# Kernel optimization log

Measured on AMD Instinct MI355X. Metric: run time of the kernel, lower is better.

## Reference

```python
import jax, jax.numpy as jnp
import numpy as np

B, C, Q, D = 64, 512, 64, 256  # D = 2 * hidden_size; similarity weight has 3*D = 768 entries


def _length_mask(key, batch, seqlen):
    # realistic padding masks: each row has a random valid prefix length in [seqlen//2, seqlen]
    lens = jax.random.randint(key, (batch,), seqlen // 2, seqlen + 1)
    return (jnp.arange(seqlen)[None, :] < lens[:, None]).astype(jnp.int32)


def setup_inputs() -> dict:
    key = jax.random.key(0)
    k1, k2, k3, k4, k5 = jax.random.split(key, 5)
    context = jax.random.normal(k1, (B, C, D), dtype=jnp.float32)
    question = jax.random.normal(k2, (B, Q, D), dtype=jnp.float32)
    context_mask = _length_mask(k3, B, C)
    question_mask = _length_mask(k4, B, Q)
    w = jax.random.normal(k5, (3 * D,), dtype=jnp.float32) * (1.0 / np.sqrt(3 * D))
    return {"context": context, "question": question,
            "context_mask": context_mask, "question_mask": question_mask, "w": w}


def reference(context, question, context_mask, question_mask, w):
    d = context.shape[-1]
    # Linear([c, q, c*q]) with no bias decomposes exactly into three terms.
    w_c, w_q, w_m = w[:d], w[d:2 * d], w[2 * d:]
    sim = ((context @ w_c)[:, :, None]                      # [B, C, 1]
           + (question @ w_q)[:, None, :]                   # [B, 1, Q]
           + jnp.einsum('bcd,bqd->bcq', context * w_m, question))  # [B, C, Q]
    neg = jnp.finfo(sim.dtype).min
    # context-to-query attention (mask question positions)
    sim_q = jnp.where(question_mask[:, None, :] != 0, sim, neg)
    a = jax.nn.softmax(sim_q, axis=2)                        # [B, C, Q]
    c2q = jnp.einsum('bcq,bqd->bcd', a, question)            # [B, C, D]
    # query-to-context attention (max over Q, mask context positions)
    sim_max = jnp.max(sim, axis=2)                           # [B, C]
    sim_max = jnp.where(context_mask != 0, sim_max, neg)
    b = jax.nn.softmax(sim_max, axis=1)                      # [B, C]
    q2c = jnp.einsum('bc,bcd->bd', b, context)[:, None, :]   # [B, 1, D]
    q2c = jnp.broadcast_to(q2c, context.shape)               # [B, C, D]
    g = jnp.concatenate([context, c2q, context * c2q, context * q2c], axis=-1)
    return g
```

## Files before the change

kernel.cpp:

```cpp
#include <hip/hip_runtime.h>
#include <hip/hip_bf16.h>
#include <float.h>

#define B_ 64
#define C_ 512
#define Q_ 64
#define D_ 256

typedef _Float16 f16x8 __attribute__((ext_vector_type(8)));
typedef float f32x4 __attribute__((ext_vector_type(4)));

union U4H8 { uint4 u; f16x8 h; };
union UH2 { _Float16 h[2]; uint32_t u; };

__device__ __forceinline__ uint32_t packh2(float a, float b) {
  UH2 v; v.h[0] = (_Float16)a; v.h[1] = (_Float16)b; return v.u;
}

__device__ __forceinline__ float wred_sum(float v) {
#pragma unroll
  for (int off = 32; off > 0; off >>= 1) v += __shfl_xor(v, off, 64);
  return v;
}
__device__ __forceinline__ float wred_max(float v) {
#pragma unroll
  for (int off = 32; off > 0; off >>= 1) v = fmaxf(v, __shfl_xor(v, off, 64));
  return v;
}

__global__ __launch_bounds__(256) void k_rowdot(const float* __restrict__ src,
                                                const float* __restrict__ wgt,
                                                float* __restrict__ out, int nrows) {
  int wv = threadIdx.x >> 6, ln = threadIdx.x & 63;
  int row = blockIdx.x * 4 + wv;
  if (row >= nrows) return;
  float4 s4 = *(const float4*)(src + (size_t)row * D_ + 4 * ln);
  float4 w4 = *(const float4*)(wgt + 4 * ln);
  float p = s4.x * w4.x + s4.y * w4.y + s4.z * w4.z + s4.w * w4.w;
  p = wred_sum(p);
  if (ln == 0) out[row] = p;
}

__global__ __launch_bounds__(256, 2) void k_main(
    const float* __restrict__ ctx, const float* __restrict__ qst,
    const int* __restrict__ qmask, const float* __restrict__ w,
    const float* __restrict__ qwq_g, float* __restrict__ g,
    float* __restrict__ simmax_g) {
  __shared__ __align__(16) ushort qraw[Q_ * D_];
  __shared__ __align__(16) ushort qT[D_ * Q_];
  __shared__ __align__(16) ushort pbuf[4][16 * Q_];
  __shared__ float qwq_l[Q_];
  __shared__ int   qml_l[Q_];

  const int bid = blockIdx.x;
  const int b = bid & 63;
  const int c0 = (bid >> 6) * 64;
  const int t = threadIdx.x;
  const int wv = t >> 6, ln = t & 63;
  const int lc = ln & 15;
  const int lg = ln >> 4;
  const int c0w = c0 + wv * 16;

  f16x8 bfrag[8];
  float cwc_p = 0.f;
  const float* crow = ctx + ((size_t)b * C_ + c0w + lc) * D_;
  float* grow0 = g + ((size_t)b * C_ + c0w + lc) * (4 * D_);
#pragma unroll
  for (int kk = 0; kk < 8; ++kk) {
    int kb = kk * 32 + lg * 8;
    float4 cv0 = *(const float4*)(crow + kb);
    float4 cv1 = *(const float4*)(crow + kb + 4);
    float4 wc0 = *(const float4*)(w + kb);
    float4 wc1 = *(const float4*)(w + kb + 4);
    float4 wm0 = *(const float4*)(w + 2 * D_ + kb);
    float4 wm1 = *(const float4*)(w + 2 * D_ + kb + 4);
    cwc_p += cv0.x * wc0.x + cv0.y * wc0.y + cv0.z * wc0.z + cv0.w * wc0.w
           + cv1.x * wc1.x + cv1.y * wc1.y + cv1.z * wc1.z + cv1.w * wc1.w;
    bfrag[kk][0] = (_Float16)(cv0.x * wm0.x);
    bfrag[kk][1] = (_Float16)(cv0.y * wm0.y);
    bfrag[kk][2] = (_Float16)(cv0.z * wm0.z);
    bfrag[kk][3] = (_Float16)(cv0.w * wm0.w);
    bfrag[kk][4] = (_Float16)(cv1.x * wm1.x);
    bfrag[kk][5] = (_Float16)(cv1.y * wm1.y);
    bfrag[kk][6] = (_Float16)(cv1.z * wm1.z);
    bfrag[kk][7] = (_Float16)(cv1.w * wm1.w);
    *(float4*)(grow0 + kb) = cv0;
    *(float4*)(grow0 + kb + 4) = cv1;
  }
  float cwc = cwc_p;
  cwc += __shfl_xor(cwc, 16, 64);
  cwc += __shfl_xor(cwc, 32, 64);

  const float* qb = qst + (size_t)b * Q_ * D_;
#pragma unroll 4
  for (int it = 0; it < 32; ++it) {
    int idx = it * 256 + t;
    int q = idx >> 7, jp = idx & 127;
    float2 v = *(const float2*)(qb + q * D_ + 2 * jp);
    int ch = jp >> 2;
    int phys = (ch & ~7) | ((ch & 7) ^ (q & 7));
    *(uint32_t*)((char*)qraw + q * 512 + phys * 16 + (jp & 3) * 4) = packh2(v.x, v.y);
  }
#pragma unroll 4
  for (int it = 0; it < 32; ++it) {
    int q = t & 63;
    int jp = (t >> 6) + 4 * it;
    float2 v = *(const float2*)(qb + q * D_ + 2 * jp);
    int d0 = 2 * jp, d1 = d0 + 1;
    UH2 h0; h0.h[0] = (_Float16)v.x;
    UH2 h1; h1.h[0] = (_Float16)v.y;
    *(ushort*)((char*)qT + d0 * 128 + (((q >> 3) ^ (d0 & 7)) << 4) + (q & 7) * 2) = (ushort)(h0.u & 0xffff);
    *(ushort*)((char*)qT + d1 * 128 + (((q >> 3) ^ (d1 & 7)) << 4) + (q & 7) * 2) = (ushort)(h1.u & 0xffff);
  }
  if (t < Q_) { qwq_l[t] = qwq_g[b * Q_ + t]; qml_l[t] = qmask[b * Q_ + t]; }
  __syncthreads();

  f32x4 sacc[4];
#pragma unroll
  for (int tq = 0; tq < 4; ++tq) sacc[tq] = f32x4{0.f, 0.f, 0.f, 0.f};
#pragma unroll
  for (int tq = 0; tq < 4; ++tq) {
    int q = 16 * tq + lc;
#pragma unroll
    for (int kk = 0; kk < 8; ++kk) {
      int ch = lg + 4 * kk;
      int phys = (ch & ~7) | ((ch & 7) ^ (q & 7));
      U4H8 a; a.u = *(const uint4*)((const char*)qraw + q * 512 + phys * 16);
      sacc[tq] = __builtin_amdgcn_mfma_f32_16x16x32_f16(a.h, bfrag[kk], sacc[tq], 0, 0, 0);
    }
  }

  float vals[4][4];
  float rmax = -FLT_MAX;
#pragma unroll
  for (int tq = 0; tq < 4; ++tq) {
    float4 qw4 = *(const float4*)(qwq_l + 16 * tq + 4 * lg);
#pragma unroll
    for (int r = 0; r < 4; ++r) {
      float qv = (r == 0) ? qw4.x : (r == 1) ? qw4.y : (r == 2) ? qw4.z : qw4.w;
      vals[tq][r] = sacc[tq][r] + cwc + qv;
      rmax = fmaxf(rmax, vals[tq][r]);
    }
  }
  rmax = fmaxf(rmax, __shfl_xor(rmax, 16, 64));
  rmax = fmaxf(rmax, __shfl_xor(rmax, 32, 64));
  if (ln < 16) simmax_g[b * C_ + c0w + lc] = rmax;

  float mmax = -FLT_MAX;
#pragma unroll
  for (int tq = 0; tq < 4; ++tq) {
    int4 qm4 = *(const int4*)(qml_l + 16 * tq + 4 * lg);
#pragma unroll
    for (int r = 0; r < 4; ++r) {
      int m = (r == 0) ? qm4.x : (r == 1) ? qm4.y : (r == 2) ? qm4.z : qm4.w;
      vals[tq][r] = m ? vals[tq][r] : -FLT_MAX;
      mmax = fmaxf(mmax, vals[tq][r]);
    }
  }
  mmax = fmaxf(mmax, __shfl_xor(mmax, 16, 64));
  mmax = fmaxf(mmax, __shfl_xor(mmax, 32, 64));
  float esum = 0.f;
#pragma unroll
  for (int tq = 0; tq < 4; ++tq)
#pragma unroll
    for (int r = 0; r < 4; ++r) {
      vals[tq][r] = __expf(vals[tq][r] - mmax);
      esum += vals[tq][r];
    }
  esum += __shfl_xor(esum, 16, 64);
  esum += __shfl_xor(esum, 32, 64);
  float inv = 1.f / esum;
#pragma unroll
  for (int tq = 0; tq < 4; ++tq) {
    uint32_t p01 = packh2(vals[tq][0] * inv, vals[tq][1] * inv);
    uint32_t p23 = packh2(vals[tq][2] * inv, vals[tq][3] * inv);
    int qb4 = 16 * tq + 4 * lg;
    int phys = ((qb4 >> 3) ^ (lc & 7));
    char* dst = (char*)pbuf[wv] + lc * 128 + phys * 16 + (qb4 & 7) * 2;
    *(uint2*)dst = uint2{p01, p23};
  }

  f16x8 pfragB[2];
#pragma unroll
  for (int ks = 0; ks < 2; ++ks) {
    int phys = (lg + 4 * ks) ^ (lc & 7);
    U4H8 a; a.u = *(const uint4*)((const char*)pbuf[wv] + lc * 128 + phys * 16);
    pfragB[ks] = a.h;
  }
  const float* crow2 = ctx + ((size_t)b * C_ + c0w + lc) * D_;
  float* grow = g + ((size_t)b * C_ + c0w + lc) * (4 * D_);
#pragma unroll 4
  for (int dt = 0; dt < 16; ++dt) {
    f32x4 acc = f32x4{0.f, 0.f, 0.f, 0.f};
#pragma unroll
    for (int ks = 0; ks < 2; ++ks) {
      int d = dt * 16 + lc;
      int phys = (lg + 4 * ks) ^ (d & 7);
      U4H8 aq; aq.u = *(const uint4*)((const char*)qT + d * 128 + phys * 16);
      acc = __builtin_amdgcn_mfma_f32_16x16x32_f16(aq.h, pfragB[ks], acc, 0, 0, 0);
    }
    int dcol = dt * 16 + 4 * lg;
    float4 cvv = *(const float4*)(crow2 + dcol);
    float4 c2qv{acc[0], acc[1], acc[2], acc[3]};
    *(float4*)(grow + D_ + dcol) = c2qv;
    float4 p2{cvv.x * c2qv.x, cvv.y * c2qv.y, cvv.z * c2qv.z, cvv.w * c2qv.w};
    *(float4*)(grow + 2 * D_ + dcol) = p2;
  }
}

__global__ __launch_bounds__(256) void k_q2c_bs(const float* __restrict__ ctx,
                                                const float* __restrict__ simmax,
                                                const int* __restrict__ cmask,
                                                float* __restrict__ part) {
  int b = blockIdx.x, ch = blockIdx.y, t = threadIdx.x;
  int wv = t >> 6, ln = t & 63;
  __shared__ float bls[C_];
  __shared__ float sred[4];
  __shared__ float ssum[4];
  float v0 = simmax[b * C_ + t], v1 = simmax[b * C_ + 256 + t];
  if (!cmask[b * C_ + t]) v0 = -FLT_MAX;
  if (!cmask[b * C_ + 256 + t]) v1 = -FLT_MAX;
  float mx = wred_max(fmaxf(v0, v1));
  if (ln == 0) sred[wv] = mx;
  __syncthreads();
  float bm = fmaxf(fmaxf(sred[0], sred[1]), fmaxf(sred[2], sred[3]));
  float e0 = __expf(v0 - bm), e1 = __expf(v1 - bm);
  float ps = wred_sum(e0 + e1);
  if (ln == 0) ssum[wv] = ps;
  __syncthreads();
  float bs = ssum[0] + ssum[1] + ssum[2] + ssum[3];
  float invbs = 1.f / bs;
  bls[t] = e0 * invbs;
  bls[256 + t] = e1 * invbs;
  __syncthreads();
  float acc = 0.f;
  int cbeg = ch * 64;
#pragma unroll 4
  for (int c = cbeg; c < cbeg + 64; ++c)
    acc += bls[c] * ctx[((size_t)b * C_ + c) * D_ + t];
  part[((size_t)b * 8 + ch) * D_ + t] = acc;
}

__global__ __launch_bounds__(256) void k_g3q(const float* __restrict__ ctx,
                                             const float* __restrict__ part,
                                             float* __restrict__ g) {
  int b = blockIdx.x, ch = blockIdx.y, t = threadIdx.x;
  __shared__ float q2c_l[D_];
  float s = 0.f;
#pragma unroll
  for (int k = 0; k < 8; ++k) s += part[((size_t)b * 8 + k) * D_ + t];
  q2c_l[t] = s;
  __syncthreads();
  int d4 = t & 63;
  int ro = t >> 6;
  float4 qv = *(const float4*)(q2c_l + 4 * d4);
#pragma unroll 4
  for (int it = 0; it < 16; ++it) {
    int c = ch * 64 + it * 4 + ro;
    float4 cv = *(const float4*)(ctx + ((size_t)b * C_ + c) * D_ + 4 * d4);
    float4 o{cv.x * qv.x, cv.y * qv.y, cv.z * qv.z, cv.w * qv.w};
    *(float4*)(g + ((size_t)b * C_ + c) * (4 * D_) + 3 * D_ + 4 * d4) = o;
  }
}

extern "C" void kernel_launch(void* const* d_in, const int* in_sizes, int n_in,
                              void* d_out, int out_size, void* d_ws, size_t ws_size,
                              hipStream_t stream) {
  const float* ctx   = (const float*)d_in[0];
  const float* qst   = (const float*)d_in[1];
  const int*   cmask = (const int*)d_in[2];
  const int*   qmask = (const int*)d_in[3];
  const float* w     = (const float*)d_in[4];
  float* g  = (float*)d_out;
  float* ws = (float*)d_ws;

  float* qwq    = ws;
  float* simmax = ws + 4096;
  float* part   = ws + 36864;

  k_rowdot<<<dim3(B_ * Q_ / 4), 256, 0, stream>>>(qst, w + D_, qwq, B_ * Q_);
  k_main<<<dim3(512), 256, 0, stream>>>(ctx, qst, qmask, w, qwq, g, simmax);
  k_q2c_bs<<<dim3(B_, 8), 256, 0, stream>>>(ctx, simmax, cmask, part);
  k_g3q<<<dim3(B_, 8), 256, 0, stream>>>(ctx, part, g);
}
```

Baseline: 66.41 us.

## Prepack swizzled fp16 question tiles once per batch and DMA them into LDS

```diff
diff --git a/kernel.cpp b/kernel.cpp
--- a/kernel.cpp
+++ b/kernel.cpp
@@ -41,11 +41,59 @@
   if (ln == 0) out[row] = p;
 }
 
+__global__ __launch_bounds__(512) void k_prepack(const float* __restrict__ qst,
+                                                 const float* __restrict__ w,
+                                                 uint32_t* __restrict__ qraw_img,
+                                                 uint32_t* __restrict__ qT_img,
+                                                 float* __restrict__ qwq) {
+  const int b = blockIdx.x;
+  const int t = threadIdx.x;
+  const float* qb = qst + (size_t)b * Q_ * D_;
+#pragma unroll
+  for (int it = 0; it < 16; ++it) {
+    int idx = it * 512 + t;
+    int q = idx >> 7, jp = idx & 127;
+    float2 v = *(const float2*)(qb + q * D_ + 2 * jp);
+    int ch = jp >> 2;
+    int phys = (ch & ~7) | ((ch & 7) ^ (q & 7));
+    qraw_img[(size_t)b * 8192 + q * 128 + phys * 4 + (jp & 3)] = packh2(v.x, v.y);
+  }
+  if (t < 256) {
+    int d = t;
+    uint32_t* dst = qT_img + (size_t)b * 8192 + d * 32;
+#pragma unroll
+    for (int qc = 0; qc < 8; ++qc) {
+      uint32_t tmp[4];
+#pragma unroll
+      for (int e = 0; e < 4; ++e) {
+        int q0 = qc * 8 + e * 2;
+        tmp[e] = packh2(qb[q0 * D_ + d], qb[(q0 + 1) * D_ + d]);
+      }
+      int pc = qc ^ (d & 7);
+      *(uint4*)(dst + pc * 4) = uint4{tmp[0], tmp[1], tmp[2], tmp[3]};
+    }
+  } else {
+    int q = (t - 256) >> 2, sl = t & 3;
+    float p = 0.f;
+#pragma unroll
+    for (int i = 0; i < 16; ++i) {
+      float4 v = *(const float4*)(qb + q * D_ + sl * 64 + i * 4);
+      float4 ww = *(const float4*)(w + D_ + sl * 64 + i * 4);
+      p += v.x * ww.x + v.y * ww.y + v.z * ww.z + v.w * ww.w;
+    }
+    p += __shfl_xor(p, 1, 64);
+    p += __shfl_xor(p, 2, 64);
+    if (sl == 0) qwq[b * Q_ + q] = p;
+  }
+}
+
+template<int IMG>
 __global__ __launch_bounds__(256, 2) void k_main(
     const float* __restrict__ ctx, const float* __restrict__ qst,
     const int* __restrict__ qmask, const float* __restrict__ w,
-    const float* __restrict__ qwq_g, float* __restrict__ g,
-    float* __restrict__ simmax_g) {
+    const float* __restrict__ qwq_g,
+    const uint32_t* __restrict__ qraw_img, const uint32_t* __restrict__ qT_img,
+    float* __restrict__ g, float* __restrict__ simmax_g) {
   __shared__ __align__(16) ushort qraw[Q_ * D_];
   __shared__ __align__(16) ushort qT[D_ * Q_];
   __shared__ __align__(16) ushort pbuf[4][16 * Q_];
@@ -60,6 +108,23 @@
   const int lc = ln & 15;
   const int lg = ln >> 4;
   const int c0w = c0 + wv * 16;
+
+  if constexpr (IMG) {
+    const uint32_t* qr_src = qraw_img + (size_t)b * 8192;
+    const uint32_t* qt_src = qT_img + (size_t)b * 8192;
+#pragma unroll
+    for (int i = 0; i < 8; ++i)
+      __builtin_amdgcn_global_load_lds(
+          (const __attribute__((address_space(1))) uint32_t*)(qr_src + i * 1024 + t * 4),
+          (__attribute__((address_space(3))) uint32_t*)((uint32_t*)qraw + i * 1024 + t * 4),
+          16, 0, 0);
+#pragma unroll
+    for (int i = 0; i < 8; ++i)
+      __builtin_amdgcn_global_load_lds(
+          (const __attribute__((address_space(1))) uint32_t*)(qt_src + i * 1024 + t * 4),
+          (__attribute__((address_space(3))) uint32_t*)((uint32_t*)qT + i * 1024 + t * 4),
+          16, 0, 0);
+  }
 
   f16x8 bfrag[8];
   float cwc_p = 0.f;
@@ -91,26 +156,28 @@
   cwc += __shfl_xor(cwc, 16, 64);
   cwc += __shfl_xor(cwc, 32, 64);
 
-  const float* qb = qst + (size_t)b * Q_ * D_;
-#pragma unroll 4
-  for (int it = 0; it < 32; ++it) {
-    int idx = it * 256 + t;
-    int q = idx >> 7, jp = idx & 127;
-    float2 v = *(const float2*)(qb + q * D_ + 2 * jp);
-    int ch = jp >> 2;
-    int phys = (ch & ~7) | ((ch & 7) ^ (q & 7));
-    *(uint32_t*)((char*)qraw + q * 512 + phys * 16 + (jp & 3) * 4) = packh2(v.x, v.y);
-  }
-#pragma unroll 4
-  for (int it = 0; it < 32; ++it) {
-    int q = t & 63;
-    int jp = (t >> 6) + 4 * it;
-    float2 v = *(const float2*)(qb + q * D_ + 2 * jp);
-    int d0 = 2 * jp, d1 = d0 + 1;
-    UH2 h0; h0.h[0] = (_Float16)v.x;
-    UH2 h1; h1.h[0] = (_Float16)v.y;
-    *(ushort*)((char*)qT + d0 * 128 + (((q >> 3) ^ (d0 & 7)) << 4) + (q & 7) * 2) = (ushort)(h0.u & 0xffff);
-    *(ushort*)((char*)qT + d1 * 128 + (((q >> 3) ^ (d1 & 7)) << 4) + (q & 7) * 2) = (ushort)(h1.u & 0xffff);
+  if constexpr (!IMG) {
+    const float* qb = qst + (size_t)b * Q_ * D_;
+#pragma unroll 4
+    for (int it = 0; it < 32; ++it) {
+      int idx = it * 256 + t;
+      int q = idx >> 7, jp = idx & 127;
+      float2 v = *(const float2*)(qb + q * D_ + 2 * jp);
+      int ch = jp >> 2;
+      int phys = (ch & ~7) | ((ch & 7) ^ (q & 7));
+      *(uint32_t*)((char*)qraw + q * 512 + phys * 16 + (jp & 3) * 4) = packh2(v.x, v.y);
+    }
+#pragma unroll 4
+    for (int it = 0; it < 32; ++it) {
+      int q = t & 63;
+      int jp = (t >> 6) + 4 * it;
+      float2 v = *(const float2*)(qb + q * D_ + 2 * jp);
+      int d0 = 2 * jp, d1 = d0 + 1;
+      UH2 h0; h0.h[0] = (_Float16)v.x;
+      UH2 h1; h1.h[0] = (_Float16)v.y;
+      *(ushort*)((char*)qT + d0 * 128 + (((q >> 3) ^ (d0 & 7)) << 4) + (q & 7) * 2) = (ushort)(h0.u & 0xffff);
+      *(ushort*)((char*)qT + d1 * 128 + (((q >> 3) ^ (d1 & 7)) << 4) + (q & 7) * 2) = (ushort)(h1.u & 0xffff);
+    }
   }
   if (t < Q_) { qwq_l[t] = qwq_g[b * Q_ + t]; qml_l[t] = qmask[b * Q_ + t]; }
   __syncthreads();
@@ -274,12 +341,22 @@
   float* g  = (float*)d_out;
   float* ws = (float*)d_ws;
 
-  float* qwq    = ws;
-  float* simmax = ws + 4096;
-  float* part   = ws + 36864;
-
-  k_rowdot<<<dim3(B_ * Q_ / 4), 256, 0, stream>>>(qst, w + D_, qwq, B_ * Q_);
-  k_main<<<dim3(512), 256, 0, stream>>>(ctx, qst, qmask, w, qwq, g, simmax);
+  float*    qwq      = ws;
+  float*    simmax   = ws + 4096;
+  float*    part     = ws + 36864;
+  uint32_t* qraw_img = (uint32_t*)(ws + 167936);
+  uint32_t* qT_img   = (uint32_t*)(ws + 692224);
+  const size_t need_bytes = (size_t)(692224 + 524288) * 4;
+
+  if (ws_size >= need_bytes) {
+    k_prepack<<<dim3(B_), 512, 0, stream>>>(qst, w, qraw_img, qT_img, qwq);
+    k_main<1><<<dim3(512), 256, 0, stream>>>(ctx, qst, qmask, w, qwq,
+                                             qraw_img, qT_img, g, simmax);
+  } else {
+    k_rowdot<<<dim3(B_ * Q_ / 4), 256, 0, stream>>>(qst, w + D_, qwq, B_ * Q_);
+    k_main<0><<<dim3(512), 256, 0, stream>>>(ctx, qst, qmask, w, qwq,
+                                             qraw_img, qT_img, g, simmax);
+  }
   k_q2c_bs<<<dim3(B_, 8), 256, 0, stream>>>(ctx, simmax, cmask, part);
   k_g3q<<<dim3(B_, 8), 256, 0, stream>>>(ctx, part, g);
 }
```

Result: faster. 63.07 us (-5.0%).
